# Kernel optimization log

Hardware: AMD Instinct MI355X
Metric: run time of the kernel (lower is better)

## Reference

```python
import jax, jax.numpy as jnp
import numpy as np

T, B, P, H = 4096, 16, 512, 512
DT_MIN, DT_MAX = 1e-3, 0.1


def setup_inputs() -> dict:
    key = jax.random.key(0)
    k_in, k_b, k_dt = jax.random.split(key, 3)
    inputs = jax.random.normal(k_in, (T, B, H), dtype=jnp.float32)
    # HiPPO-diag init: a_diag = -sqrt(2n+1)*sqrt(2n+3); log_neg_a = log(-a_diag)
    n = jnp.arange(P, dtype=jnp.float32)
    log_neg_a = jnp.log(jnp.sqrt(2 * n + 1) * jnp.sqrt(2 * n + 3))
    b = jax.random.normal(k_b, (P, H), dtype=jnp.float32) * 0.01
    log_dt = jax.random.uniform(k_dt, (P,), dtype=jnp.float32) * (
        np.float32(np.log(DT_MAX)) - np.float32(np.log(DT_MIN))
    ) + np.float32(np.log(DT_MIN))
    return {"inputs": inputs, "log_neg_a": log_neg_a, "b": b, "log_dt": log_dt}


def reference(inputs, log_neg_a, b, log_dt):
    # Discretization (matches torch module exactly, including extra dt factor)
    dt = jnp.exp(log_dt)                       # [P]
    a = -jnp.exp(log_neg_a)                    # [P]
    a_bar = jnp.exp(dt * a)                    # [P]
    b_bar = ((a_bar - 1.0) / a)[:, None] * b * dt[:, None]  # [P, H]

    # Precompute driving term for all timesteps: u_t @ b_bar.T -> [T, B, P]
    bu = jnp.einsum("tbh,ph->tbp", inputs, b_bar)

    batch = inputs.shape[1]
    z0 = jnp.zeros((batch, a_bar.shape[0]), dtype=inputs.dtype)

    def step(z, bu_t):
        z = a_bar[None, :] * z + bu_t
        return z, z

    _, zs = jax.lax.scan(step, z0, bu)  # [T, B, P]
    return zs
```

## Files before the change

kernel.cpp:

```cpp
#include <hip/hip_runtime.h>
#include <math.h>

#define T_DIM 4096
#define B_DIM 16
#define P_DIM 512
#define H_DIM 512
#define M_DIM (T_DIM * B_DIM)
#define BP (B_DIM * P_DIM)
#define BP4 (BP / 4)
#define P4 (P_DIM / 4)

#define KBYTES (H_DIM * 2)
#define BK 64

#define CLEN_F 8
#define CHUNKS_F (T_DIM / CLEN_F)
#define GROUP 16
#define NGROUPS (CHUNKS_F / GROUP)
#define CLEN_S 64
#define CHUNKS_S (T_DIM / CLEN_S)

#define SCALE_B 1048576.0f
#define INV_SCALE_B (1.0f / 1048576.0f)

typedef _Float16 f16x8 __attribute__((ext_vector_type(8)));
typedef float f32x4 __attribute__((ext_vector_type(4)));

__device__ __forceinline__ void gload16(const void* g, void* l) {
    __builtin_amdgcn_global_load_lds(
        (const __attribute__((address_space(1))) void*)(uintptr_t)g,
        (__attribute__((address_space(3))) void*)(uint32_t)(uintptr_t)l,
        16, 0, 0);
}

__global__ __launch_bounds__(256) void precompute_kernel(
    const float* __restrict__ log_neg_a,
    const float* __restrict__ b,
    const float* __restrict__ log_dt,
    float* __restrict__ b_bar,
    _Float16* __restrict__ b_bar16,
    float* __restrict__ a_bar,
    float* __restrict__ aL8,
    float* __restrict__ aL128,
    float* __restrict__ aL64,
    float* __restrict__ aL8pow,
    int write16) {
    int idx = blockIdx.x * blockDim.x + threadIdx.x;
    if (idx >= P_DIM * H_DIM) return;
    int p = idx >> 9;
    float dt = expf(log_dt[p]);
    float a  = -expf(log_neg_a[p]);
    float x  = dt * a;
    float scale = (expm1f(x) / a) * dt;
    float bb = scale * b[idx];
    b_bar[idx] = bb;
    if (write16) b_bar16[idx] = (_Float16)(bb * SCALE_B);
    if ((idx & (H_DIM - 1)) == 0) {
        a_bar[p] = expf(x);
        float l8 = expf(x * 8.0f);
        aL8[p]   = l8;
        aL128[p] = expf(x * 128.0f);
        aL64[p]  = expf(x * 64.0f);
        float pw = 1.0f;
        for (int j = 0; j < GROUP; ++j) {
            aL8pow[j * P_DIM + p] = pw;
            pw *= l8;
        }
    }
}

__global__ __launch_bounds__(256) void gemm_regA_scan_kernel(
    const float* __restrict__ A,
    const char* __restrict__ B16,
    const float* __restrict__ a_bar,
    float* __restrict__ Cout,
    float* __restrict__ carry) {
    __shared__ char As[128 * BK * 2];
    __shared__ char Bs[128 * BK * 2];

    const int tid  = threadIdx.x;
    const int lane = tid & 63;
    const int wid  = tid >> 6;
    const int rowBase = blockIdx.y * 128;
    const int colBase = blockIdx.x * 128;

    const int arow  = tid >> 3;
    const int slot8 = tid & 7;
    const float* gA = A + (size_t)(rowBase + arow) * H_DIM + slot8 * 8;
    const int adst  = arow * 128 + ((slot8 ^ (arow & 7)) << 4);

    const int srow = tid >> 3;
    const int scolb = ((tid & 7) << 4) ^ ((srow & 7) << 4);
    const char* gB = B16 + (size_t)(colBase + srow) * KBYTES + scolb;

    f32x4 acc[4][4];
#pragma unroll
    for (int m2 = 0; m2 < 4; ++m2)
#pragma unroll
        for (int n2 = 0; n2 < 4; ++n2)
            acc[m2][n2] = (f32x4){0.f, 0.f, 0.f, 0.f};

    const int wr = wid >> 1;
    const int wc = wid & 1;

    for (int kt = 0; kt < H_DIM / BK; ++kt) {
#pragma unroll
        for (int i = 0; i < 4; ++i)
            gload16(gB + (size_t)i * 32 * KBYTES, Bs + (i * 256 + wid * 64) * 16);
        float4 a0[4], a1[4];
#pragma unroll
        for (int i = 0; i < 4; ++i) {
            const float* src = gA + (size_t)i * 32 * H_DIM;
            a0[i] = *(const float4*)(src);
            a1[i] = *(const float4*)(src + 4);
        }
#pragma unroll
        for (int i = 0; i < 4; ++i) {
            f16x8 v;
            v[0] = (_Float16)a0[i].x; v[1] = (_Float16)a0[i].y;
            v[2] = (_Float16)a0[i].z; v[3] = (_Float16)a0[i].w;
            v[4] = (_Float16)a1[i].x; v[5] = (_Float16)a1[i].y;
            v[6] = (_Float16)a1[i].z; v[7] = (_Float16)a1[i].w;
            *(f16x8*)(As + i * 32 * 128 + adst) = v;
        }
        gA += BK;
        gB += BK * 2;
        __syncthreads();

#pragma unroll
        for (int kk = 0; kk < 2; ++kk) {
            const int kbyte = kk * 64 + ((lane >> 4) << 4);
            f16x8 af[4], bf[4];
#pragma unroll
            for (int m2 = 0; m2 < 4; ++m2) {
                int row = wr * 64 + m2 * 16 + (lane & 15);
                af[m2] = *(const f16x8*)(As + row * 128 + (kbyte ^ ((row & 7) << 4)));
            }
#pragma unroll
            for (int n2 = 0; n2 < 4; ++n2) {
                int col = wc * 64 + n2 * 16 + (lane & 15);
                bf[n2] = *(const f16x8*)(Bs + col * 128 + (kbyte ^ ((col & 7) << 4)));
            }
#pragma unroll
            for (int m2 = 0; m2 < 4; ++m2)
#pragma unroll
                for (int n2 = 0; n2 < 4; ++n2)
                    acc[m2][n2] = __builtin_amdgcn_mfma_f32_16x16x32_f16(
                        af[m2], bf[n2], acc[m2][n2], 0, 0, 0);
        }
        __syncthreads();
    }

    float* lds_z = (float*)As;
    const int pl = wc * 64 + (lane & 15);

    float ab[4];
#pragma unroll
    for (int n2 = 0; n2 < 4; ++n2) ab[n2] = a_bar[colBase + pl + n2 * 16];

    if (wr == 0) {
#pragma unroll
        for (int n2 = 0; n2 < 4; ++n2)
#pragma unroll
            for (int r = 0; r < 4; ++r) {
                float z = 0.f;
#pragma unroll
                for (int m2 = 0; m2 < 4; ++m2) {
                    z = fmaf(ab[n2], z, acc[m2][n2][r]);
                    acc[m2][n2][r] = z;
                }
                lds_z[((lane >> 4) * 4 + r) * 128 + pl + n2 * 16] = z;
            }
    }
    __syncthreads();
    if (wr == 1) {
#pragma unroll
        for (int n2 = 0; n2 < 4; ++n2)
#pragma unroll
            for (int r = 0; r < 4; ++r) {
                float z = lds_z[((lane >> 4) * 4 + r) * 128 + pl + n2 * 16];
#pragma unroll
                for (int m2 = 0; m2 < 4; ++m2) {
                    z = fmaf(ab[n2], z, acc[m2][n2][r]);
                    acc[m2][n2][r] = z;
                }
                int b = (lane >> 4) * 4 + r;
                carry[(size_t)blockIdx.y * BP + b * P_DIM + colBase + pl + n2 * 16] =
                    z * INV_SCALE_B;
            }
    }

#pragma unroll
    for (int m2 = 0; m2 < 4; ++m2) {
#pragma unroll
        for (int r = 0; r < 4; ++r) {
            size_t row = (size_t)(rowBase + wr * 64 + m2 * 16 + (lane >> 4) * 4 + r);
            float* po = Cout + row * P_DIM + colBase + wc * 64 + (lane & 15);
#pragma unroll
            for (int n2 = 0; n2 < 4; ++n2)
                po[n2 * 16] = acc[m2][n2][r] * INV_SCALE_B;
        }
    }
}

__global__ __launch_bounds__(256) void group_scan_kernel(
    const float4* __restrict__ carry,
    const float4* __restrict__ aL8_4,
    float4* __restrict__ y,
    float4* __restrict__ G) {
    int tid = blockIdx.x * blockDim.x + threadIdx.x;
    int bp4 = tid & (BP4 - 1);
    int g = tid >> 11;
    float4 ab = aL8_4[bp4 & (P4 - 1)];
    float4 z = make_float4(0.f, 0.f, 0.f, 0.f);
#pragma unroll
    for (int j = 0; j < GROUP; ++j) {
        size_t c = (size_t)(g * GROUP + j) * BP4 + bp4;
        y[c] = z;
        float4 v = carry[c];
        z.x = fmaf(ab.x, z.x, v.x);
        z.y = fmaf(ab.y, z.y, v.y);
        z.z = fmaf(ab.z, z.z, v.z);
        z.w = fmaf(ab.w, z.w, v.w);
    }
    G[(size_t)g * BP4 + bp4] = z;
}

__global__ __launch_bounds__(256) void gcarry_scan_kernel(
    const float* __restrict__ G,
    const float* __restrict__ aL128,
    float* __restrict__ gz) {
    int bp = blockIdx.x * blockDim.x + threadIdx.x;
    float aL = aL128[bp & (P_DIM - 1)];
    float z = 0.f;
#pragma unroll
    for (int g = 0; g < NGROUPS; ++g) {
        gz[g * BP + bp] = z;
        z = fmaf(aL, z, G[g * BP + bp]);
    }
}

__global__ __launch_bounds__(256) void fixup8_kernel(
    float4* __restrict__ zio,
    const float4* __restrict__ a_bar4,
    const float4* __restrict__ y,
    const float4* __restrict__ gz,
    const float4* __restrict__ aL8pow4) {
    int tid = blockIdx.x * blockDim.x + threadIdx.x;
    int bp4 = tid & (BP4 - 1);
    int c = (tid >> 11) + 1;
    int p4 = bp4 & (P4 - 1);
    int g = c >> 4;
    int j = c & (GROUP - 1);
    float4 ab = a_bar4[p4];
    float4 pw = aL8pow4[j * P4 + p4];
    float4 yy = y[(size_t)c * BP4 + bp4];
    float4 gzz = gz[(size_t)g * BP4 + bp4];
    float4 zin;
    zin.x = fmaf(pw.x, gzz.x, yy.x);
    zin.y = fmaf(pw.y, gzz.y, yy.y);
    zin.z = fmaf(pw.z, gzz.z, yy.z);
    zin.w = fmaf(pw.w, gzz.w, yy.w);
    float4 f = ab;
    size_t base = (size_t)c * CLEN_F * BP4 + bp4;
#pragma unroll
    for (int i = 0; i < CLEN_F; ++i) {
        size_t off = base + (size_t)i * BP4;
        float4 v = zio[off];
        v.x = fmaf(f.x, zin.x, v.x);
        v.y = fmaf(f.y, zin.y, v.y);
        v.z = fmaf(f.z, zin.z, v.z);
        v.w = fmaf(f.w, zin.w, v.w);
        zio[off] = v;
        f.x *= ab.x;
        f.y *= ab.y;
        f.z *= ab.z;
        f.w *= ab.w;
    }
}

#define BM 128
#define BN 128
#define BKF 16
__global__ __launch_bounds__(256) void gemm_kernel(
    const float* __restrict__ A,
    const float* __restrict__ Bm,
    float* __restrict__ Cout) {
    __shared__ float As[BM][BKF + 1];
    __shared__ float Bs[BN][BKF + 4];
    const int K = H_DIM;
    const int N = P_DIM;
    int tid = threadIdx.x;
    int tx = tid & 15;
    int ty = tid >> 4;
    int rowBase = blockIdx.y * BM;
    int colBase = blockIdx.x * BN;
    float acc[8][8];
#pragma unroll
    for (int i = 0; i < 8; ++i)
#pragma unroll
        for (int j = 0; j < 8; ++j) acc[i][j] = 0.f;
    for (int kt = 0; kt < K; kt += BKF) {
#pragma unroll
        for (int l = 0; l < 2; ++l) {
            int fl = tid * 2 + l;
            int row = fl >> 2;
            int kq = fl & 3;
            float4 av = *reinterpret_cast<const float4*>(
                &A[(size_t)(rowBase + row) * K + kt + kq * 4]);
            As[row][kq * 4 + 0] = av.x;
            As[row][kq * 4 + 1] = av.y;
            As[row][kq * 4 + 2] = av.z;
            As[row][kq * 4 + 3] = av.w;
            float4 bv = *reinterpret_cast<const float4*>(
                &Bm[(size_t)(colBase + row) * K + kt + kq * 4]);
            *reinterpret_cast<float4*>(&Bs[row][kq * 4]) = bv;
        }
        __syncthreads();
#pragma unroll
        for (int k = 0; k < BKF; ++k) {
            float af[8], bf[8];
#pragma unroll
            for (int i = 0; i < 8; ++i) af[i] = As[ty * 8 + i][k];
#pragma unroll
            for (int j = 0; j < 8; ++j) bf[j] = Bs[tx + 16 * j][k];
#pragma unroll
            for (int i = 0; i < 8; ++i)
#pragma unroll
                for (int j = 0; j < 8; ++j)
                    acc[i][j] = fmaf(af[i], bf[j], acc[i][j]);
        }
        __syncthreads();
    }
#pragma unroll
    for (int i = 0; i < 8; ++i) {
        size_t r = (size_t)(rowBase + ty * 8 + i);
#pragma unroll
        for (int j = 0; j < 8; ++j)
            Cout[r * N + colBase + tx + 16 * j] = acc[i][j];
    }
}

__global__ __launch_bounds__(256) void scan_local_kernel(
    float4* __restrict__ zio,
    const float4* __restrict__ a_bar4,
    float4* __restrict__ carry) {
    int tid = blockIdx.x * blockDim.x + threadIdx.x;
    int bp4 = tid & (BP4 - 1);
    int c = tid >> 11;
    float4 ab = a_bar4[bp4 & (P4 - 1)];
    size_t base = (size_t)c * CLEN_S * BP4 + bp4;
    float4 z = make_float4(0.f, 0.f, 0.f, 0.f);
    for (int i = 0; i < CLEN_S; ++i) {
        size_t off = base + (size_t)i * BP4;
        float4 v = zio[off];
        z.x = fmaf(ab.x, z.x, v.x);
        z.y = fmaf(ab.y, z.y, v.y);
        z.z = fmaf(ab.z, z.z, v.z);
        z.w = fmaf(ab.w, z.w, v.w);
        zio[off] = z;
    }
    carry[tid] = z;
}

__global__ __launch_bounds__(256) void carry_scan_kernel(
    const float4* __restrict__ carry,
    const float4* __restrict__ aL4,
    float4* __restrict__ z_in,
    int nchunks) {
    int bp4 = blockIdx.x * blockDim.x + threadIdx.x;
    float4 aL = aL4[bp4 & (P4 - 1)];
    float4 z = make_float4(0.f, 0.f, 0.f, 0.f);
    for (int c = 0; c < nchunks; ++c) {
        z_in[(size_t)c * BP4 + bp4] = z;
        float4 v = carry[(size_t)c * BP4 + bp4];
        z.x = fmaf(aL.x, z.x, v.x);
        z.y = fmaf(aL.y, z.y, v.y);
        z.z = fmaf(aL.z, z.z, v.z);
        z.w = fmaf(aL.w, z.w, v.w);
    }
}

__global__ __launch_bounds__(256) void fixup_kernel(
    float4* __restrict__ zio,
    const float4* __restrict__ a_bar4,
    const float4* __restrict__ z_in,
    int clen) {
    int tid = blockIdx.x * blockDim.x + threadIdx.x;
    int bp4 = tid & (BP4 - 1);
    int c = (tid >> 11) + 1;
    float4 ab = a_bar4[bp4 & (P4 - 1)];
    float4 zin = z_in[(size_t)c * BP4 + bp4];
    float4 f = ab;
    size_t base = (size_t)c * clen * BP4 + bp4;
    for (int i = 0; i < clen; ++i) {
        size_t off = base + (size_t)i * BP4;
        float4 v = zio[off];
        v.x = fmaf(f.x, zin.x, v.x);
        v.y = fmaf(f.y, zin.y, v.y);
        v.z = fmaf(f.z, zin.z, v.z);
        v.w = fmaf(f.w, zin.w, v.w);
        zio[off] = v;
        f.x *= ab.x;
        f.y *= ab.y;
        f.z *= ab.z;
        f.w *= ab.w;
    }
}

extern "C" void kernel_launch(void* const* d_in, const int* in_sizes, int n_in,
                              void* d_out, int out_size, void* d_ws, size_t ws_size,
                              hipStream_t stream) {
    const float* inputs    = (const float*)d_in[0];
    const float* log_neg_a = (const float*)d_in[1];
    const float* b         = (const float*)d_in[2];
    const float* log_dt    = (const float*)d_in[3];
    float* out = (float*)d_out;
    float* ws  = (float*)d_ws;

    float* b_bar   = ws;
    float* a_bar   = b_bar + P_DIM * H_DIM;
    float* aL8     = a_bar + P_DIM;
    float* aL128   = aL8 + P_DIM;
    float* aL64    = aL128 + P_DIM;
    float* aL8pow  = aL64 + P_DIM;
    float* carry   = aL8pow + GROUP * P_DIM;
    float* y       = carry + (size_t)CHUNKS_F * BP;
    float* G       = y + (size_t)CHUNKS_F * BP;
    float* gz      = G + (size_t)NGROUPS * BP;
    float* tail    = gz + (size_t)NGROUPS * BP;
    _Float16* b_bar16 = (_Float16*)tail;

    size_t ws_need = (size_t)((char*)(b_bar16 + (size_t)P_DIM * H_DIM) - (char*)ws);
    int fast = (ws_size >= ws_need);

    precompute_kernel<<<(P_DIM * H_DIM) / 256, 256, 0, stream>>>(
        log_neg_a, b, log_dt, b_bar, b_bar16, a_bar, aL8, aL128, aL64, aL8pow, fast);

    if (fast) {
        dim3 ggrid(P_DIM / 128, M_DIM / 128);
        gemm_regA_scan_kernel<<<ggrid, 256, 0, stream>>>(
            inputs, (const char*)b_bar16, a_bar, out, carry);

        group_scan_kernel<<<(NGROUPS * BP4) / 256, 256, 0, stream>>>(
            (const float4*)carry, (const float4*)aL8, (float4*)y, (float4*)G);

        gcarry_scan_kernel<<<BP / 256, 256, 0, stream>>>(G, aL128, gz);

        fixup8_kernel<<<((CHUNKS_F - 1) * BP4) / 256, 256, 0, stream>>>(
            (float4*)out, (const float4*)a_bar, (const float4*)y,
            (const float4*)gz, (const float4*)aL8pow);
    } else {
        dim3 ggrid(P_DIM / BN, M_DIM / BM);
        gemm_kernel<<<ggrid, 256, 0, stream>>>(inputs, b_bar, out);

        scan_local_kernel<<<(CHUNKS_S * BP4) / 256, 256, 0, stream>>>(
            (float4*)out, (const float4*)a_bar, (float4*)carry);

        carry_scan_kernel<<<BP4 / 256, 256, 0, stream>>>(
            (const float4*)carry, (const float4*)aL64, (float4*)y, CHUNKS_S);

        fixup_kernel<<<((CHUNKS_S - 1) * BP4) / 256, 256, 0, stream>>>(
            (float4*)out, (const float4*)a_bar, (const float4*)y, CLEN_S);
    }
}
```

Before: 163.8 us.

## Double-buffer GEMM LDS tiles and remap block order for XCD locality

The GEMM+local-scan kernel now uses two LDS buffers per operand. The next K-tile's global loads for A (into registers) and B (async to LDS) are issued before the current tile's MFMAs, and the f16 conversion of A is stored after them, so memory latency overlaps with compute and one barrier per iteration is dropped. The launch becomes a 1D grid whose block index is remapped, so that blocks sharing A rows land on the same XCD (blockIdx mod 8) for L2 reuse. LDS use doubles to 64KB per block, which may reduce occupancy.

```diff
diff --git a/kernel.cpp b/kernel.cpp
--- a/kernel.cpp
+++ b/kernel.cpp
@@ -12,6 +12,7 @@
 
 #define KBYTES (H_DIM * 2)
 #define BK 64
+#define NKT (H_DIM / BK)
 
 #define CLEN_F 8
 #define CHUNKS_F (T_DIM / CLEN_F)
@@ -69,29 +70,35 @@
     }
 }
 
-__global__ __launch_bounds__(256) void gemm_regA_scan_kernel(
+__global__ __launch_bounds__(256) void gemm_db_scan_kernel(
     const float* __restrict__ A,
     const char* __restrict__ B16,
     const float* __restrict__ a_bar,
     float* __restrict__ Cout,
     float* __restrict__ carry) {
-    __shared__ char As[128 * BK * 2];
-    __shared__ char Bs[128 * BK * 2];
+    __shared__ char As[2][128 * BK * 2];
+    __shared__ char Bs[2][128 * BK * 2];
 
     const int tid  = threadIdx.x;
     const int lane = tid & 63;
     const int wid  = tid >> 6;
-    const int rowBase = blockIdx.y * 128;
-    const int colBase = blockIdx.x * 128;
+
+    const int l   = blockIdx.x;
+    const int k8  = l & 7;
+    const int j   = l >> 3;
+    const int by  = k8 * 64 + (j >> 2);
+    const int bx  = j & 3;
+    const int rowBase = by * 128;
+    const int colBase = bx * 128;
 
     const int arow  = tid >> 3;
     const int slot8 = tid & 7;
     const float* gA = A + (size_t)(rowBase + arow) * H_DIM + slot8 * 8;
     const int adst  = arow * 128 + ((slot8 ^ (arow & 7)) << 4);
 
-    const int srow = tid >> 3;
+    const int srow  = tid >> 3;
     const int scolb = ((tid & 7) << 4) ^ ((srow & 7) << 4);
-    const char* gB = B16 + (size_t)(colBase + srow) * KBYTES + scolb;
+    const char* gB  = B16 + (size_t)(colBase + srow) * KBYTES + scolb;
 
     f32x4 acc[4][4];
 #pragma unroll
@@ -103,30 +110,42 @@
     const int wr = wid >> 1;
     const int wc = wid & 1;
 
-    for (int kt = 0; kt < H_DIM / BK; ++kt) {
-#pragma unroll
-        for (int i = 0; i < 4; ++i)
-            gload16(gB + (size_t)i * 32 * KBYTES, Bs + (i * 256 + wid * 64) * 16);
-        float4 a0[4], a1[4];
-#pragma unroll
-        for (int i = 0; i < 4; ++i) {
-            const float* src = gA + (size_t)i * 32 * H_DIM;
-            a0[i] = *(const float4*)(src);
-            a1[i] = *(const float4*)(src + 4);
-        }
-#pragma unroll
-        for (int i = 0; i < 4; ++i) {
-            f16x8 v;
-            v[0] = (_Float16)a0[i].x; v[1] = (_Float16)a0[i].y;
-            v[2] = (_Float16)a0[i].z; v[3] = (_Float16)a0[i].w;
-            v[4] = (_Float16)a1[i].x; v[5] = (_Float16)a1[i].y;
-            v[6] = (_Float16)a1[i].z; v[7] = (_Float16)a1[i].w;
-            *(f16x8*)(As + i * 32 * 128 + adst) = v;
-        }
-        gA += BK;
-        gB += BK * 2;
-        __syncthreads();
-
+    float4 p0[4], p1[4];
+#pragma unroll
+    for (int i = 0; i < 4; ++i) {
+        const float* src = gA + (size_t)i * 32 * H_DIM;
+        p0[i] = *(const float4*)(src);
+        p1[i] = *(const float4*)(src + 4);
+    }
+#pragma unroll
+    for (int i = 0; i < 4; ++i)
+        gload16(gB + (size_t)i * 32 * KBYTES, Bs[0] + (i * 256 + wid * 64) * 16);
+#pragma unroll
+    for (int i = 0; i < 4; ++i) {
+        f16x8 v;
+        v[0] = (_Float16)p0[i].x; v[1] = (_Float16)p0[i].y;
+        v[2] = (_Float16)p0[i].z; v[3] = (_Float16)p0[i].w;
+        v[4] = (_Float16)p1[i].x; v[5] = (_Float16)p1[i].y;
+        v[6] = (_Float16)p1[i].z; v[7] = (_Float16)p1[i].w;
+        *(f16x8*)(As[0] + i * 32 * 128 + adst) = v;
+    }
+    __syncthreads();
+
+#pragma unroll
+    for (int kt = 0; kt < NKT; ++kt) {
+        const int cur = kt & 1;
+        if (kt < NKT - 1) {
+#pragma unroll
+            for (int i = 0; i < 4; ++i) {
+                const float* src = gA + (size_t)(kt + 1) * BK + (size_t)i * 32 * H_DIM;
+                p0[i] = *(const float4*)(src);
+                p1[i] = *(const float4*)(src + 4);
+            }
+#pragma unroll
+            for (int i = 0; i < 4; ++i)
+                gload16(gB + (size_t)(kt + 1) * BK * 2 + (size_t)i * 32 * KBYTES,
+                        Bs[cur ^ 1] + (i * 256 + wid * 64) * 16);
+        }
 #pragma unroll
         for (int kk = 0; kk < 2; ++kk) {
             const int kbyte = kk * 64 + ((lane >> 4) << 4);
@@ -134,12 +153,12 @@
 #pragma unroll
             for (int m2 = 0; m2 < 4; ++m2) {
                 int row = wr * 64 + m2 * 16 + (lane & 15);
-                af[m2] = *(const f16x8*)(As + row * 128 + (kbyte ^ ((row & 7) << 4)));
+                af[m2] = *(const f16x8*)(As[cur] + row * 128 + (kbyte ^ ((row & 7) << 4)));
             }
 #pragma unroll
             for (int n2 = 0; n2 < 4; ++n2) {
                 int col = wc * 64 + n2 * 16 + (lane & 15);
-                bf[n2] = *(const f16x8*)(Bs + col * 128 + (kbyte ^ ((col & 7) << 4)));
+                bf[n2] = *(const f16x8*)(Bs[cur] + col * 128 + (kbyte ^ ((col & 7) << 4)));
             }
 #pragma unroll
             for (int m2 = 0; m2 < 4; ++m2)
@@ -148,10 +167,21 @@
                     acc[m2][n2] = __builtin_amdgcn_mfma_f32_16x16x32_f16(
                         af[m2], bf[n2], acc[m2][n2], 0, 0, 0);
         }
+        if (kt < NKT - 1) {
+#pragma unroll
+            for (int i = 0; i < 4; ++i) {
+                f16x8 v;
+                v[0] = (_Float16)p0[i].x; v[1] = (_Float16)p0[i].y;
+                v[2] = (_Float16)p0[i].z; v[3] = (_Float16)p0[i].w;
+                v[4] = (_Float16)p1[i].x; v[5] = (_Float16)p1[i].y;
+                v[6] = (_Float16)p1[i].z; v[7] = (_Float16)p1[i].w;
+                *(f16x8*)(As[cur ^ 1] + i * 32 * 128 + adst) = v;
+            }
+        }
         __syncthreads();
     }
 
-    float* lds_z = (float*)As;
+    float* lds_z = (float*)As[0];
     const int pl = wc * 64 + (lane & 15);
 
     float ab[4];
@@ -185,7 +215,7 @@
                     acc[m2][n2][r] = z;
                 }
                 int b = (lane >> 4) * 4 + r;
-                carry[(size_t)blockIdx.y * BP + b * P_DIM + colBase + pl + n2 * 16] =
+                carry[(size_t)by * BP + b * P_DIM + colBase + pl + n2 * 16] =
                     z * INV_SCALE_B;
             }
     }
@@ -438,8 +468,7 @@
         log_neg_a, b, log_dt, b_bar, b_bar16, a_bar, aL8, aL128, aL64, aL8pow, fast);
 
     if (fast) {
-        dim3 ggrid(P_DIM / 128, M_DIM / 128);
-        gemm_regA_scan_kernel<<<ggrid, 256, 0, stream>>>(
+        gemm_db_scan_kernel<<<2048, 256, 0, stream>>>(
             inputs, (const char*)b_bar16, a_bar, out, carry);
 
         group_scan_kernel<<<(NGROUPS * BP4) / 256, 256, 0, stream>>>(
```

Result: no change. 163.8 us (-0.1%).
